# Optimization experiments

Hardware: AMD Instinct MI355X
Metric: run time of the kernel (lower is better)

Reference implementation:

```python
import jax, jax.numpy as jnp
import numpy as np

B, IN, OUT, R, G = 1024, 4096, 4096, 16, 16
N_GROUPS = IN * OUT // G  # 1048576


def setup_inputs() -> dict:
    key = jax.random.key(0)
    k1, k2, k3, k4, k5 = jax.random.split(key, 5)
    x = jax.random.normal(k1, (B, IN), dtype=jnp.float32)
    # packed 4-bit weights: each int holds two nibbles (low | high<<4), values 0..255
    qweight = jax.random.randint(k2, (N_GROUPS, G // 2), 0, 256, dtype=jnp.int32)
    # positive per-group scale (original stores abs-max as fp16, used as fp32)
    scale_factor = jax.random.uniform(k3, (N_GROUPS, 1), dtype=jnp.float32, minval=0.01, maxval=1.0)
    # kaiming-normal-ish init for lora_a; lora_b nonzero for a non-degenerate baseline
    lora_a = jax.random.normal(k4, (R, IN), dtype=jnp.float32) * np.sqrt(2.0 / IN).astype(np.float32)
    lora_b = jax.random.normal(k5, (OUT, R), dtype=jnp.float32) * 0.01
    alpha = jnp.ones((1,), dtype=jnp.float32)
    return {"x": x, "qweight": qweight, "scale_factor": scale_factor,
            "lora_a": lora_a, "lora_b": lora_b, "alpha": alpha}


def _dequantize_4bit(qweight, scale_factor):
    # qweight: [n_groups, G/2] int32 packed nibbles; scale: [n_groups, 1]
    g, half = qweight.shape
    lo = qweight & 15            # even positions
    hi = (qweight >> 4) & 15     # odd positions
    q8 = jnp.stack([lo, hi], axis=-1).reshape(g, half * 2)  # interleave -> [n_groups, G]
    x_norm = q8.astype(jnp.float32) / 15.0
    return x_norm * 2.0 * scale_factor - scale_factor       # [n_groups, G]


def reference(x, qweight, scale_factor, lora_a, lora_b, alpha):
    # dequantize and view as (in_features, -1), matching weight.view(x.shape[1], -1)
    weight = _dequantize_4bit(qweight, scale_factor).reshape(x.shape[1], -1)  # [IN, OUT]
    base = jnp.einsum('bi,oi->bo', x, weight)  # F.linear(x, weight) = x @ weight.T
    lora = alpha * jnp.einsum('br,or->bo', jnp.einsum('bi,ri->br', x, lora_a), lora_b)
    return base + lora
```

## Files before the change

### kernel.cpp

```cpp
#include <hip/hip_runtime.h>

typedef __attribute__((ext_vector_type(2))) _Float16 h2;
typedef __attribute__((ext_vector_type(2))) __fp16 p2;
typedef __attribute__((ext_vector_type(8))) _Float16 f16x8;
typedef __attribute__((ext_vector_type(4))) float fv4;
typedef __attribute__((ext_vector_type(4))) int iv4;
typedef __attribute__((ext_vector_type(2))) int iv2;
typedef unsigned int u32;

#define K_IN 4096
#define N_OUT 4096
#define KE 4160

__global__ __launch_bounds__(256) void x_prep(const float* __restrict__ x,
                                              const float* __restrict__ la,
                                              _Float16* __restrict__ xh) {
    int b = blockIdx.x;
    int t = threadIdx.x;
    const fv4* xp = (const fv4*)(x + (size_t)b * K_IN);
    _Float16* xr = xh + (size_t)b * KE;
    fv4 xv[4];
#pragma unroll
    for (int j = 0; j < 4; ++j) xv[j] = xp[t + j * 256];
#pragma unroll
    for (int j = 0; j < 4; ++j) {
        union { p2 h[2]; iv2 v; } u;
        u.h[0] = __builtin_amdgcn_cvt_pkrtz(xv[j].x, xv[j].y);
        u.h[1] = __builtin_amdgcn_cvt_pkrtz(xv[j].z, xv[j].w);
        *(iv2*)(xr + (size_t)(t + j * 256) * 4) = u.v;
    }
    float acc[16];
#pragma unroll
    for (int r = 0; r < 16; ++r) {
        const fv4* ap = (const fv4*)(la + (size_t)r * K_IN);
        float s = 0.f;
#pragma unroll
        for (int j = 0; j < 4; ++j) {
            fv4 av = ap[t + j * 256];
            s = fmaf(xv[j].x, av.x, s);
            s = fmaf(xv[j].y, av.y, s);
            s = fmaf(xv[j].z, av.z, s);
            s = fmaf(xv[j].w, av.w, s);
        }
        acc[r] = s;
    }
#pragma unroll
    for (int r = 0; r < 16; ++r) {
#pragma unroll
        for (int off = 1; off < 64; off <<= 1)
            acc[r] += __shfl_xor(acc[r], off);
    }
    __shared__ float red[4][16];
    int lane = t & 63, w = t >> 6;
    if (lane < 16) red[w][lane] = acc[lane];
    __syncthreads();
    if (t < 16)
        xr[4096 + t] = (_Float16)(red[0][t] + red[1][t] + red[2][t] + red[3][t]);
    else if (t < 64)
        xr[4112 + (t - 16)] = (_Float16)0.f;
}

__global__ __launch_bounds__(256) void w_dequant2(const int* __restrict__ qw,
                                                  const float* __restrict__ sc,
                                                  const float* __restrict__ lb,
                                                  const float* __restrict__ alphap,
                                                  _Float16* __restrict__ Wh) {
    int bid = blockIdx.x;
    int t = threadIdx.x;
    if (bid < 4096) {
        int grp = bid * 256 + t;
        int o = grp >> 8;
        int i0 = (grp & 255) << 4;
        const int* qp = qw + (size_t)grp * 8;
        iv4 q0 = *(const iv4*)qp;
        iv4 q1 = *(const iv4*)(qp + 4);
        float s = sc[grp];
        _Float16 c0h = (_Float16)(s * (2.0f / 15.0f));
        _Float16 c1h = (_Float16)(-s);
        h2 c0 = {c0h, c0h}, c1 = {c1h, c1h};
        h2 m1024 = {(_Float16)-1024.f, (_Float16)-1024.f};
        union { h2 h[4]; iv4 v; } o0, o1;
        int vals[8] = {q0.x, q0.y, q0.z, q0.w, q1.x, q1.y, q1.z, q1.w};
#pragma unroll
        for (int e = 0; e < 8; ++e) {
            unsigned wv = (unsigned)vals[e];
            unsigned qb = (wv & 15u) | ((wv & 0xF0u) << 12) | 0x64006400u;
            h2 qh;
            __builtin_memcpy(&qh, &qb, 4);
            h2 r = (qh + m1024) * c0 + c1;
            if (e < 4) o0.h[e] = r; else o1.h[e - 4] = r;
        }
        _Float16* wp = Wh + (size_t)o * KE + i0;
        *(iv4*)(wp) = o0.v;
        *(iv4*)(wp + 8) = o1.v;
    } else {
        int c = (bid - 4096) * 256 + t;
        int o = c >> 3, jj = c & 7;
        union { p2 h[4]; iv4 v; } u;
        u.v = iv4{0, 0, 0, 0};
        if (jj < 2) {
            float al = alphap[0];
            const float* wp = lb + (size_t)o * 16 + jj * 8;
#pragma unroll
            for (int e = 0; e < 4; ++e)
                u.h[e] = __builtin_amdgcn_cvt_pkrtz(al * wp[2 * e], al * wp[2 * e + 1]);
        }
        *(iv4*)(Wh + (size_t)o * KE + 4096 + jj * 8) = u.v;
    }
}

__global__ __launch_bounds__(512, 1) void qlora_gemm2(
        const _Float16* __restrict__ xh, const _Float16* __restrict__ Wh,
        float* __restrict__ out)
{
    __shared__ __align__(16) char lds[131072];

    int bid = blockIdx.x;
    int xcd = bid & 7, j = bid >> 3;
    int by = j & 7, bx = xcd * 4 + (j >> 3);
    int bm0 = by << 7, bn0 = bx << 7;

    int t = threadIdx.x;
    int lane = t & 63;
    int wid = t >> 6;
    int kg = wid & 1, wn = (wid >> 1) & 1, wm = wid >> 2;
    int rl = lane & 15, hq = lane >> 4;

    int sr = t >> 4;
    int sp = t & 15;
    int sg = sp ^ (sr & 15);
    const char* asrc[4];
    const char* bsrc[4];
#pragma unroll
    for (int i = 0; i < 4; ++i) {
        asrc[i] = (const char*)(xh + (size_t)(bm0 + i * 32 + sr) * KE) + sg * 16;
        bsrc[i] = (const char*)(Wh + (size_t)(bn0 + i * 32 + sr) * KE) + sg * 16;
    }
    int tr = t >> 3;
    int tg = (t & 7) ^ (tr & 7);
    const char* atail[2];
    const char* btail[2];
#pragma unroll
    for (int i = 0; i < 2; ++i) {
        atail[i] = (const char*)(xh + (size_t)(bm0 + i * 64 + tr) * KE + 4096) + tg * 16;
        btail[i] = (const char*)(Wh + (size_t)(bn0 + i * 64 + tr) * KE + 4096) + tg * 16;
    }

    auto GLOAD = [&](int ts, int buf) {
        char* Ad = lds + buf * 32768;
        char* Bd = lds + 65536 + buf * 32768;
        size_t off = (size_t)ts * 256;
#pragma unroll
        for (int i = 0; i < 4; ++i) {
            __builtin_amdgcn_global_load_lds(
                (const __attribute__((address_space(1))) u32*)(asrc[i] + off),
                (__attribute__((address_space(3))) u32*)(Ad + i * 8192 + t * 16), 16, 0, 0);
            __builtin_amdgcn_global_load_lds(
                (const __attribute__((address_space(1))) u32*)(bsrc[i] + off),
                (__attribute__((address_space(3))) u32*)(Bd + i * 8192 + t * 16), 16, 0, 0);
        }
    };
    auto GLOAD_TAIL = [&](int buf) {
        char* Ad = lds + buf * 32768;
        char* Bd = lds + 65536 + buf * 32768;
#pragma unroll
        for (int i = 0; i < 2; ++i) {
            __builtin_amdgcn_global_load_lds(
                (const __attribute__((address_space(1))) u32*)(atail[i]),
                (__attribute__((address_space(3))) u32*)(Ad + i * 8192 + t * 16), 16, 0, 0);
            __builtin_amdgcn_global_load_lds(
                (const __attribute__((address_space(1))) u32*)(btail[i]),
                (__attribute__((address_space(3))) u32*)(Bd + i * 8192 + t * 16), 16, 0, 0);
        }
    };

    fv4 acc[4][4];
#pragma unroll
    for (int m = 0; m < 4; ++m)
#pragma unroll
        for (int n = 0; n < 4; ++n)
            acc[m][n] = fv4{0.f, 0.f, 0.f, 0.f};

    auto COMPUTE = [&](int buf) {
        const char* As = lds + buf * 32768;
        const char* Bs = lds + 65536 + buf * 32768;
#pragma unroll
        for (int s = 0; s < 2; ++s) {
            f16x8 a[4], b[4];
            int gk = kg * 8 + s * 4 + hq;
            int gs = (gk ^ rl) << 4;
#pragma unroll
            for (int m = 0; m < 4; ++m)
                a[m] = *(const f16x8*)(As + (wm * 64 + m * 16 + rl) * 256 + gs);
#pragma unroll
            for (int n = 0; n < 4; ++n)
                b[n] = *(const f16x8*)(Bs + (wn * 64 + n * 16 + rl) * 256 + gs);
            __builtin_amdgcn_s_setprio(1);
#pragma unroll
            for (int m = 0; m < 4; ++m)
#pragma unroll
                for (int n = 0; n < 4; ++n)
                    acc[m][n] = __builtin_amdgcn_mfma_f32_16x16x32_f16(
                        a[m], b[n], acc[m][n], 0, 0, 0);
            __builtin_amdgcn_s_setprio(0);
        }
    };
    auto COMPUTE_TAIL = [&](int buf) {
        const char* As = lds + buf * 32768;
        const char* Bs = lds + 65536 + buf * 32768;
        f16x8 a[4], b[4];
        int gk = kg * 4 + hq;
        int gs = (gk ^ (rl & 7)) << 4;
#pragma unroll
        for (int m = 0; m < 4; ++m)
            a[m] = *(const f16x8*)(As + (wm * 64 + m * 16 + rl) * 128 + gs);
#pragma unroll
        for (int n = 0; n < 4; ++n)
            b[n] = *(const f16x8*)(Bs + (wn * 64 + n * 16 + rl) * 128 + gs);
        __builtin_amdgcn_s_setprio(1);
#pragma unroll
        for (int m = 0; m < 4; ++m)
#pragma unroll
            for (int n = 0; n < 4; ++n)
                acc[m][n] = __builtin_amdgcn_mfma_f32_16x16x32_f16(
                    a[m], b[n], acc[m][n], 0, 0, 0);
        __builtin_amdgcn_s_setprio(0);
    };

    GLOAD(0, 0);
    asm volatile("s_waitcnt vmcnt(0)" ::: "memory");
    __builtin_amdgcn_s_barrier();
    __builtin_amdgcn_sched_barrier(0);

#pragma unroll 1
    for (int ts = 0; ts < 32; ++ts) {
        if (ts < 31) GLOAD(ts + 1, (ts + 1) & 1);
        else         GLOAD_TAIL(0);
        COMPUTE(ts & 1);
        asm volatile("s_waitcnt vmcnt(0) lgkmcnt(0)" ::: "memory");
        __builtin_amdgcn_s_barrier();
        __builtin_amdgcn_sched_barrier(0);
    }
    COMPUTE_TAIL(0);

    __syncthreads();
    if (kg == 1) {
        char* dmp = lds + (wm * 2 + wn) * 16384;
#pragma unroll
        for (int m = 0; m < 4; ++m)
#pragma unroll
            for (int n = 0; n < 4; ++n)
                *(fv4*)(dmp + (m * 4 + n) * 1024 + lane * 16) = acc[m][n];
    }
    __syncthreads();
    if (kg == 0) {
        const char* dmp = lds + (wm * 2 + wn) * 16384;
#pragma unroll
        for (int m = 0; m < 4; ++m) {
            int row0 = bm0 + wm * 64 + m * 16 + hq * 4;
#pragma unroll
            for (int n = 0; n < 4; ++n) {
                fv4 p = *(const fv4*)(dmp + (m * 4 + n) * 1024 + lane * 16);
                fv4 v = acc[m][n];
                v.x += p.x; v.y += p.y; v.z += p.z; v.w += p.w;
                int col = bn0 + wn * 64 + n * 16 + rl;
#pragma unroll
                for (int r = 0; r < 4; ++r)
                    out[(size_t)(row0 + r) * N_OUT + col] = v[r];
            }
        }
    }
}

extern "C" void kernel_launch(void* const* d_in, const int* in_sizes, int n_in,
                              void* d_out, int out_size, void* d_ws, size_t ws_size,
                              hipStream_t stream) {
    const float* x  = (const float*)d_in[0];
    const int*   qw = (const int*)d_in[1];
    const float* sc = (const float*)d_in[2];
    const float* la = (const float*)d_in[3];
    const float* lb = (const float*)d_in[4];
    const float* al = (const float*)d_in[5];
    float* out = (float*)d_out;

    const size_t WH_BYTES = (size_t)N_OUT * KE * 2;
    _Float16* Wh = (_Float16*)d_ws;
    _Float16* xh = (_Float16*)((char*)d_ws + WH_BYTES);
    (void)ws_size; (void)n_in; (void)in_sizes; (void)out_size;

    x_prep<<<1024, 256, 0, stream>>>(x, la, xh);
    w_dequant2<<<4224, 256, 0, stream>>>(qw, sc, lb, al, Wh);
    qlora_gemm2<<<256, 512, 0, stream>>>(xh, Wh, out);
}
```

Baseline: 73.13 us.

## Merge prep kernels and switch GEMM to triple-buffered 64-wide K pipeline

Folds the x conversion/LoRA-A projection and weight dequant into one launch, removing a kernel boundary. The GEMM now loads 64-element K slices into a three-stage LDS ring with two tiles in flight and partial vmcnt waits, replacing the 128-wide double buffer. This also removes the separate tail path, since 4160 divides evenly into 65 slices. It trades twice as many barriers per K for deeper prefetch and less LDS (96KB), which risks more synchronization overhead.

```diff
diff --git a/kernel.cpp b/kernel.cpp
--- a/kernel.cpp
+++ b/kernel.cpp
@@ -12,63 +12,59 @@
 #define N_OUT 4096
 #define KE 4160
 
-__global__ __launch_bounds__(256) void x_prep(const float* __restrict__ x,
-                                              const float* __restrict__ la,
-                                              _Float16* __restrict__ xh) {
-    int b = blockIdx.x;
-    int t = threadIdx.x;
-    const fv4* xp = (const fv4*)(x + (size_t)b * K_IN);
-    _Float16* xr = xh + (size_t)b * KE;
-    fv4 xv[4];
-#pragma unroll
-    for (int j = 0; j < 4; ++j) xv[j] = xp[t + j * 256];
-#pragma unroll
-    for (int j = 0; j < 4; ++j) {
-        union { p2 h[2]; iv2 v; } u;
-        u.h[0] = __builtin_amdgcn_cvt_pkrtz(xv[j].x, xv[j].y);
-        u.h[1] = __builtin_amdgcn_cvt_pkrtz(xv[j].z, xv[j].w);
-        *(iv2*)(xr + (size_t)(t + j * 256) * 4) = u.v;
-    }
-    float acc[16];
-#pragma unroll
-    for (int r = 0; r < 16; ++r) {
-        const fv4* ap = (const fv4*)(la + (size_t)r * K_IN);
-        float s = 0.f;
-#pragma unroll
-        for (int j = 0; j < 4; ++j) {
-            fv4 av = ap[t + j * 256];
-            s = fmaf(xv[j].x, av.x, s);
-            s = fmaf(xv[j].y, av.y, s);
-            s = fmaf(xv[j].z, av.z, s);
-            s = fmaf(xv[j].w, av.w, s);
-        }
-        acc[r] = s;
-    }
-#pragma unroll
-    for (int r = 0; r < 16; ++r) {
-#pragma unroll
-        for (int off = 1; off < 64; off <<= 1)
-            acc[r] += __shfl_xor(acc[r], off);
-    }
-    __shared__ float red[4][16];
-    int lane = t & 63, w = t >> 6;
-    if (lane < 16) red[w][lane] = acc[lane];
-    __syncthreads();
-    if (t < 16)
-        xr[4096 + t] = (_Float16)(red[0][t] + red[1][t] + red[2][t] + red[3][t]);
-    else if (t < 64)
-        xr[4112 + (t - 16)] = (_Float16)0.f;
-}
-
-__global__ __launch_bounds__(256) void w_dequant2(const int* __restrict__ qw,
-                                                  const float* __restrict__ sc,
-                                                  const float* __restrict__ lb,
-                                                  const float* __restrict__ alphap,
-                                                  _Float16* __restrict__ Wh) {
+__global__ __launch_bounds__(256) void prep_all(
+        const float* __restrict__ x, const float* __restrict__ la,
+        const int* __restrict__ qw, const float* __restrict__ sc,
+        const float* __restrict__ lb, const float* __restrict__ alphap,
+        _Float16* __restrict__ xh, _Float16* __restrict__ Wh)
+{
     int bid = blockIdx.x;
     int t = threadIdx.x;
-    if (bid < 4096) {
-        int grp = bid * 256 + t;
+    if (bid < 1024) {
+        int b = bid;
+        const fv4* xp = (const fv4*)(x + (size_t)b * K_IN);
+        _Float16* xr = xh + (size_t)b * KE;
+        fv4 xv[4];
+#pragma unroll
+        for (int j = 0; j < 4; ++j) xv[j] = xp[t + j * 256];
+#pragma unroll
+        for (int j = 0; j < 4; ++j) {
+            union { p2 h[2]; iv2 v; } u;
+            u.h[0] = __builtin_amdgcn_cvt_pkrtz(xv[j].x, xv[j].y);
+            u.h[1] = __builtin_amdgcn_cvt_pkrtz(xv[j].z, xv[j].w);
+            *(iv2*)(xr + (size_t)(t + j * 256) * 4) = u.v;
+        }
+        float acc[16];
+#pragma unroll
+        for (int r = 0; r < 16; ++r) {
+            const fv4* ap = (const fv4*)(la + (size_t)r * K_IN);
+            float s = 0.f;
+#pragma unroll
+            for (int j = 0; j < 4; ++j) {
+                fv4 av = ap[t + j * 256];
+                s = fmaf(xv[j].x, av.x, s);
+                s = fmaf(xv[j].y, av.y, s);
+                s = fmaf(xv[j].z, av.z, s);
+                s = fmaf(xv[j].w, av.w, s);
+            }
+            acc[r] = s;
+        }
+#pragma unroll
+        for (int r = 0; r < 16; ++r) {
+#pragma unroll
+            for (int off = 1; off < 64; off <<= 1)
+                acc[r] += __shfl_xor(acc[r], off);
+        }
+        __shared__ float red[4][16];
+        int lane = t & 63, w = t >> 6;
+        if (lane < 16) red[w][lane] = acc[lane];
+        __syncthreads();
+        if (t < 16)
+            xr[4096 + t] = (_Float16)(red[0][t] + red[1][t] + red[2][t] + red[3][t]);
+        else if (t < 64)
+            xr[4112 + (t - 16)] = (_Float16)0.f;
+    } else if (bid < 5120) {
+        int grp = (bid - 1024) * 256 + t;
         int o = grp >> 8;
         int i0 = (grp & 255) << 4;
         const int* qp = qw + (size_t)grp * 8;
@@ -94,7 +90,7 @@
         *(iv4*)(wp) = o0.v;
         *(iv4*)(wp + 8) = o1.v;
     } else {
-        int c = (bid - 4096) * 256 + t;
+        int c = (bid - 5120) * 256 + t;
         int o = c >> 3, jj = c & 7;
         union { p2 h[4]; iv4 v; } u;
         u.v = iv4{0, 0, 0, 0};
@@ -113,7 +109,7 @@
         const _Float16* __restrict__ xh, const _Float16* __restrict__ Wh,
         float* __restrict__ out)
 {
-    __shared__ __align__(16) char lds[131072];
+    __shared__ __align__(16) char lds[98304];
 
     int bid = blockIdx.x;
     int xcd = bid & 7, j = bid >> 3;
@@ -126,32 +122,23 @@
     int kg = wid & 1, wn = (wid >> 1) & 1, wm = wid >> 2;
     int rl = lane & 15, hq = lane >> 4;
 
-    int sr = t >> 4;
-    int sp = t & 15;
-    int sg = sp ^ (sr & 15);
-    const char* asrc[4];
-    const char* bsrc[4];
-#pragma unroll
-    for (int i = 0; i < 4; ++i) {
-        asrc[i] = (const char*)(xh + (size_t)(bm0 + i * 32 + sr) * KE) + sg * 16;
-        bsrc[i] = (const char*)(Wh + (size_t)(bn0 + i * 32 + sr) * KE) + sg * 16;
-    }
-    int tr = t >> 3;
-    int tg = (t & 7) ^ (tr & 7);
-    const char* atail[2];
-    const char* btail[2];
+    int sr = t >> 3;
+    int sp = t & 7;
+    int sg = sp ^ (sr & 7);
+    const char* asrc[2];
+    const char* bsrc[2];
 #pragma unroll
     for (int i = 0; i < 2; ++i) {
-        atail[i] = (const char*)(xh + (size_t)(bm0 + i * 64 + tr) * KE + 4096) + tg * 16;
-        btail[i] = (const char*)(Wh + (size_t)(bn0 + i * 64 + tr) * KE + 4096) + tg * 16;
+        asrc[i] = (const char*)(xh + (size_t)(bm0 + i * 64 + sr) * KE) + sg * 16;
+        bsrc[i] = (const char*)(Wh + (size_t)(bn0 + i * 64 + sr) * KE) + sg * 16;
     }
 
     auto GLOAD = [&](int ts, int buf) {
         char* Ad = lds + buf * 32768;
-        char* Bd = lds + 65536 + buf * 32768;
-        size_t off = (size_t)ts * 256;
-#pragma unroll
-        for (int i = 0; i < 4; ++i) {
+        char* Bd = lds + buf * 32768 + 16384;
+        size_t off = (size_t)ts * 128;
+#pragma unroll
+        for (int i = 0; i < 2; ++i) {
             __builtin_amdgcn_global_load_lds(
                 (const __attribute__((address_space(1))) u32*)(asrc[i] + off),
                 (__attribute__((address_space(3))) u32*)(Ad + i * 8192 + t * 16), 16, 0, 0);
@@ -160,19 +147,6 @@
                 (__attribute__((address_space(3))) u32*)(Bd + i * 8192 + t * 16), 16, 0, 0);
         }
     };
-    auto GLOAD_TAIL = [&](int buf) {
-        char* Ad = lds + buf * 32768;
-        char* Bd = lds + 65536 + buf * 32768;
-#pragma unroll
-        for (int i = 0; i < 2; ++i) {
-            __builtin_amdgcn_global_load_lds(
-                (const __attribute__((address_space(1))) u32*)(atail[i]),
-                (__attribute__((address_space(3))) u32*)(Ad + i * 8192 + t * 16), 16, 0, 0);
-            __builtin_amdgcn_global_load_lds(
-                (const __attribute__((address_space(1))) u32*)(btail[i]),
-                (__attribute__((address_space(3))) u32*)(Bd + i * 8192 + t * 16), 16, 0, 0);
-        }
-    };
 
     fv4 acc[4][4];
 #pragma unroll
@@ -183,31 +157,7 @@
 
     auto COMPUTE = [&](int buf) {
         const char* As = lds + buf * 32768;
-        const char* Bs = lds + 65536 + buf * 32768;
-#pragma unroll
-        for (int s = 0; s < 2; ++s) {
-            f16x8 a[4], b[4];
-            int gk = kg * 8 + s * 4 + hq;
-            int gs = (gk ^ rl) << 4;
-#pragma unroll
-            for (int m = 0; m < 4; ++m)
-                a[m] = *(const f16x8*)(As + (wm * 64 + m * 16 + rl) * 256 + gs);
-#pragma unroll
-            for (int n = 0; n < 4; ++n)
-                b[n] = *(const f16x8*)(Bs + (wn * 64 + n * 16 + rl) * 256 + gs);
-            __builtin_amdgcn_s_setprio(1);
-#pragma unroll
-            for (int m = 0; m < 4; ++m)
-#pragma unroll
-                for (int n = 0; n < 4; ++n)
-                    acc[m][n] = __builtin_amdgcn_mfma_f32_16x16x32_f16(
-                        a[m], b[n], acc[m][n], 0, 0, 0);
-            __builtin_amdgcn_s_setprio(0);
-        }
-    };
-    auto COMPUTE_TAIL = [&](int buf) {
-        const char* As = lds + buf * 32768;
-        const char* Bs = lds + 65536 + buf * 32768;
+        const char* Bs = lds + buf * 32768 + 16384;
         f16x8 a[4], b[4];
         int gk = kg * 4 + hq;
         int gs = (gk ^ (rl & 7)) << 4;
@@ -228,20 +178,25 @@
     };
 
     GLOAD(0, 0);
-    asm volatile("s_waitcnt vmcnt(0)" ::: "memory");
+    GLOAD(1, 1);
+    asm volatile("s_waitcnt vmcnt(4)" ::: "memory");
     __builtin_amdgcn_s_barrier();
     __builtin_amdgcn_sched_barrier(0);
 
 #pragma unroll 1
-    for (int ts = 0; ts < 32; ++ts) {
-        if (ts < 31) GLOAD(ts + 1, (ts + 1) & 1);
-        else         GLOAD_TAIL(0);
-        COMPUTE(ts & 1);
-        asm volatile("s_waitcnt vmcnt(0) lgkmcnt(0)" ::: "memory");
-        __builtin_amdgcn_s_barrier();
-        __builtin_amdgcn_sched_barrier(0);
-    }
-    COMPUTE_TAIL(0);
+    for (int ts = 0; ts < 65; ++ts) {
+        if (ts <= 62) GLOAD(ts + 2, (ts + 2) % 3);
+        COMPUTE(ts % 3);
+        if (ts <= 62) {
+            asm volatile("s_waitcnt vmcnt(4)" ::: "memory");
+            __builtin_amdgcn_s_barrier();
+            __builtin_amdgcn_sched_barrier(0);
+        } else if (ts == 63) {
+            asm volatile("s_waitcnt vmcnt(0)" ::: "memory");
+            __builtin_amdgcn_s_barrier();
+            __builtin_amdgcn_sched_barrier(0);
+        }
+    }
 
     __syncthreads();
     if (kg == 1) {
@@ -288,7 +243,6 @@
     _Float16* xh = (_Float16*)((char*)d_ws + WH_BYTES);
     (void)ws_size; (void)n_in; (void)in_sizes; (void)out_size;
 
-    x_prep<<<1024, 256, 0, stream>>>(x, la, xh);
-    w_dequant2<<<4224, 256, 0, stream>>>(qw, sc, lb, al, Wh);
+    prep_all<<<5248, 256, 0, stream>>>(x, la, qw, sc, lb, al, xh, Wh);
     qlora_gemm2<<<256, 512, 0, stream>>>(xh, Wh, out);
 }
```

Result: faster. 69.75 us (-4.6%).
